# Kernel tuning notes

Measured on AMD Instinct MI355X. Metric: run time of the kernel, lower is better.

## Reference

```python
import jax, jax.numpy as jnp
import numpy as np

B, N_DEC, M_ENC, D, U = 16, 256, 256, 256, 256

def setup_inputs() -> dict:
    key = jax.random.key(0)
    ks = jax.random.split(key, 6)
    scale = 1.0 / np.sqrt(D)
    return {
        "encoder_output": jax.random.normal(ks[0], (B, M_ENC, D), dtype=jnp.float32),
        "decoder_output": jax.random.normal(ks[1], (B, N_DEC, D), dtype=jnp.float32),
        "W1": jax.random.normal(ks[2], (D, U), dtype=jnp.float32) * scale,
        "b1": jnp.zeros((U,), dtype=jnp.float32),
        "W2": jax.random.normal(ks[3], (D, U), dtype=jnp.float32) * scale,
        "b2": jnp.zeros((U,), dtype=jnp.float32),
        "v_w": jax.random.normal(ks[4], (U, 1), dtype=jnp.float32) * (1.0 / np.sqrt(U)),
        "v_b": jnp.zeros((1,), dtype=jnp.float32),
    }

def reference(encoder_output, decoder_output, W1, b1, W2, b2, v_w, v_b):
    # Project once per sequence, then broadcast (faithful to Dense on expanded dims):
    # enc_proj: [B, M, U], dec_proj: [B, N, U]
    enc_proj = jnp.einsum('bmd,du->bmu', encoder_output, W1) + b1
    dec_proj = jnp.einsum('bnd,du->bnu', decoder_output, W2) + b2
    # score: [B, N, M, U] = tanh(enc_proj[:,None,:,:] + dec_proj[:,:,None,:])
    score = jnp.tanh(enc_proj[:, None, :, :] + dec_proj[:, :, None, :])
    # logits: [B, N, M, 1]; softmax over encoder axis (axis=2)
    logits = jnp.einsum('bnmu,uo->bnmo', score, v_w) + v_b
    attention_weights = jax.nn.softmax(logits, axis=2)
    # context: sum over M of weights * encoder_output -> [B, N, D]
    context_vector = jnp.einsum('bnmo,bmd->bnd', attention_weights, encoder_output)
    return context_vector, attention_weights
```

## Files before the change

kernel.cpp:

```cpp
#include <hip/hip_runtime.h>


constexpr float KSC   = 2.8853900817779268f;
constexpr float LOG2E = 1.4426950408889634f;
constexpr float S16   = 1.52587890625e-05f;
constexpr float LSC   = -3.0517578125e-05f;

struct F4 { float v[4]; };
__device__ __forceinline__ F4 ld4(const float* p) {
    float4 t = *(const float4*)p;
    F4 r; r.v[0] = t.x; r.v[1] = t.y; r.v[2] = t.z; r.v[3] = t.w; return r;
}
__device__ __forceinline__ float rcp_clamp(float v) {
    float r = __builtin_amdgcn_rcpf(v);
    return fminf(fmaxf(r, -1e4f), 1e4f);
}

__global__ __launch_bounds__(256) void proj_kernel(
    const float* __restrict__ enc, const float* __restrict__ dec,
    const float* __restrict__ W1,  const float* __restrict__ b1,
    const float* __restrict__ W2,  const float* __restrict__ b2,
    const float* __restrict__ vw,
    float* __restrict__ encQ, float* __restrict__ decE)
{
    __shared__ float Xs[64][33];
    __shared__ float Ws[64][68];

    const int tid = threadIdx.x;
    const int tm = tid & 15, tu = tid >> 4;
    const int u0   = blockIdx.x * 64;
    const int row0 = blockIdx.y * 32;
    const bool is_enc = row0 < 4096;
    const float* X    = is_enc ? enc : dec;
    const float* W    = is_enc ? W1  : W2;
    const float* bias = is_enc ? b1  : b2;
    const int rb = is_enc ? row0 : row0 - 4096;

    float acc[2][4] = {};
    for (int kt = 0; kt < 256; kt += 64) {
        __syncthreads();
        #pragma unroll
        for (int i = 0; i < 2; ++i) {
            const int f = tid + (i << 8);
            const int row = f >> 4, kq = (f & 15) << 2;
            F4 x = ld4(&X[(rb + row) * 256 + kt + kq]);
            Xs[kq + 0][row] = x.v[0];
            Xs[kq + 1][row] = x.v[1];
            Xs[kq + 2][row] = x.v[2];
            Xs[kq + 3][row] = x.v[3];
        }
        #pragma unroll
        for (int i = 0; i < 4; ++i) {
            const int f = tid + (i << 8);
            const int kk = f >> 4, uq = (f & 15) << 2;
            *(float4*)&Ws[kk][uq] = *(const float4*)&W[(kt + kk) * 256 + u0 + uq];
        }
        __syncthreads();
        #pragma unroll 8
        for (int k = 0; k < 64; ++k) {
            const float xa0 = Xs[k][(tm << 1) | 0];
            const float xa1 = Xs[k][(tm << 1) | 1];
            const F4 wa = ld4(&Ws[k][tu << 2]);
            #pragma unroll
            for (int j = 0; j < 4; ++j) {
                acc[0][j] = fmaf(xa0, wa.v[j], acc[0][j]);
                acc[1][j] = fmaf(xa1, wa.v[j], acc[1][j]);
            }
        }
    }

    const int ucol = u0 + (tu << 2);
    const F4 bb = ld4(&bias[ucol]);
    if (is_enc) {
        const int b  = rb >> 8;
        const int m0 = (rb & 255) + (tm << 1);
        const int uq = ucol >> 2;
        #pragma unroll
        for (int i = 0; i < 2; ++i) {
            float4 o;
            o.x = __builtin_amdgcn_exp2f(fmaf(KSC, acc[i][0] + bb.v[0], -16.f));
            o.y = __builtin_amdgcn_exp2f(fmaf(KSC, acc[i][1] + bb.v[1], -16.f));
            o.z = __builtin_amdgcn_exp2f(fmaf(KSC, acc[i][2] + bb.v[2], -16.f));
            o.w = __builtin_amdgcn_exp2f(fmaf(KSC, acc[i][3] + bb.v[3], -16.f));
            *(float4*)&encQ[b * 65536 + uq * 1024 + (m0 + i) * 4] = o;
        }
    } else {
        const F4 vv = ld4(&vw[ucol]);
        float rv[4];
        #pragma unroll
        for (int j = 0; j < 4; ++j) rv[j] = rcp_clamp(vv.v[j]);
        const int r0 = rb + (tm << 1);
        #pragma unroll
        for (int i = 0; i < 2; ++i) {
            float4 o;
            o.x = __builtin_amdgcn_exp2f(KSC * (acc[i][0] + bb.v[0])) * rv[0];
            o.y = __builtin_amdgcn_exp2f(KSC * (acc[i][1] + bb.v[1])) * rv[1];
            o.z = __builtin_amdgcn_exp2f(KSC * (acc[i][2] + bb.v[2])) * rv[2];
            o.w = __builtin_amdgcn_exp2f(KSC * (acc[i][3] + bb.v[3])) * rv[3];
            *(float4*)&decE[(r0 + i) * 256 + ucol] = o;
        }
    }
}

__global__ __launch_bounds__(512) void logit_kernel(
    const float* __restrict__ encQ,
    const float* __restrict__ decE,
    const float* __restrict__ vw,
    float* __restrict__ logits)
{
    __shared__ float dsD[8][256];
    __shared__ float vcs[256];

    const int tid = threadIdx.x;
    const int b   = blockIdx.y;
    const int n0  = blockIdx.x << 3;
    const int h   = tid >> 8;
    const int m   = tid & 255;
    const int t0  = h << 2;

    {
        const float* dsrc = decE + (b * 256 + n0) * 256;
        #pragma unroll
        for (int i = 0; i < 4; ++i)
            ((float*)dsD)[tid + (i << 9)] = dsrc[tid + (i << 9)];
        if (tid < 256) vcs[tid] = S16 * rcp_clamp(vw[tid]);
    }
    __syncthreads();

    const float* ep = encQ + b * 65536 + (m << 2);
    F4 Ea = ld4(ep);
    F4 Eb = ld4(ep + 1024);
    ep += 2048;

    float acc[4] = {};

    #pragma unroll 4
    for (int o = 0; o < 32; ++o) {
        const F4 Ena = ld4(ep);
        const F4 Enb = ld4(ep + 1024);
        ep += 2048;
        const int u0 = o << 3;
        const F4 ca = ld4(&vcs[u0]);
        const F4 cb = ld4(&vcs[u0 + 4]);
        #pragma unroll
        for (int c = 0; c < 4; ++c) {
            const F4 da = ld4(&dsD[t0 + c][u0]);
            const F4 db = ld4(&dsD[t0 + c][u0 + 4]);
            const float z0 = fmaf(Ea.v[0], da.v[0], ca.v[0]);
            const float z1 = fmaf(Ea.v[1], da.v[1], ca.v[1]);
            const float z2 = fmaf(Ea.v[2], da.v[2], ca.v[2]);
            const float z3 = fmaf(Ea.v[3], da.v[3], ca.v[3]);
            const float y0 = fmaf(Eb.v[0], db.v[0], cb.v[0]);
            const float y1 = fmaf(Eb.v[1], db.v[1], cb.v[1]);
            const float y2 = fmaf(Eb.v[2], db.v[2], cb.v[2]);
            const float y3 = fmaf(Eb.v[3], db.v[3], cb.v[3]);
            const float pz01 = z0 * z1, pz23 = z2 * z3;
            const float py01 = y0 * y1, py23 = y2 * y3;
            const float nz = fmaf(z0 + z1, pz23, (z2 + z3) * pz01);
            const float ny = fmaf(y0 + y1, py23, (y2 + y3) * py01);
            const float pz = pz01 * pz23, py = py01 * py23;
            const float num = fmaf(nz, py, ny * pz);
            acc[c] = fmaf(num, __builtin_amdgcn_rcpf(pz * py), acc[c]);
        }
        Ea = Ena; Eb = Enb;
    }

    #pragma unroll
    for (int c = 0; c < 4; ++c)
        logits[(b * 256 + n0 + t0 + c) * 256 + m] = acc[c] * LSC;
}

__global__ __launch_bounds__(512) void smctx_kernel(
    const float* __restrict__ enc,
    float* __restrict__ out_attn,
    float* __restrict__ out_ctx)
{
    __shared__ float attn_s[8][256];
    __shared__ float redm[8][4], reds[8][4];

    const int tid = threadIdx.x;
    const int b   = blockIdx.y;
    const int n0  = blockIdx.x << 3;
    const int h   = tid >> 8;
    const int m   = tid & 255;
    const int t0  = h << 2;

    float l[4];
    #pragma unroll
    for (int c = 0; c < 4; ++c)
        l[c] = out_attn[(b * 256 + n0 + t0 + c) * 256 + m];

    const int lane = tid & 63, wq = (tid >> 6) & 3;
    #pragma unroll
    for (int c = 0; c < 4; ++c) {
        float x = l[c];
        #pragma unroll
        for (int off = 32; off > 0; off >>= 1)
            x = fmaxf(x, __shfl_xor(x, off));
        if (lane == 0) redm[t0 + c][wq] = x;
    }
    __syncthreads();
    float p[4];
    #pragma unroll
    for (int c = 0; c < 4; ++c) {
        const float mx = fmaxf(fmaxf(redm[t0 + c][0], redm[t0 + c][1]),
                               fmaxf(redm[t0 + c][2], redm[t0 + c][3]));
        p[c] = __builtin_amdgcn_exp2f((l[c] - mx) * LOG2E);
    }
    #pragma unroll
    for (int c = 0; c < 4; ++c) {
        float x = p[c];
        #pragma unroll
        for (int off = 32; off > 0; off >>= 1)
            x += __shfl_xor(x, off);
        if (lane == 0) reds[t0 + c][wq] = x;
    }
    __syncthreads();
    #pragma unroll
    for (int c = 0; c < 4; ++c) {
        const float s = (reds[t0 + c][0] + reds[t0 + c][1])
                      + (reds[t0 + c][2] + reds[t0 + c][3]);
        const float w = p[c] * __builtin_amdgcn_rcpf(s);
        attn_s[t0 + c][m] = w;
        out_attn[(b * 256 + n0 + t0 + c) * 256 + m] = w;
    }
    __syncthreads();

    const float* eb = enc + b * 65536 + m;
    float cx[4] = {};
    #pragma unroll 4
    for (int mm = 0; mm < 256; mm += 4) {
        const float g0 = eb[(mm + 0) << 8];
        const float g1 = eb[(mm + 1) << 8];
        const float g2 = eb[(mm + 2) << 8];
        const float g3 = eb[(mm + 3) << 8];
        #pragma unroll
        for (int c = 0; c < 4; ++c) {
            const F4 aq = ld4(&attn_s[t0 + c][mm]);
            cx[c] = fmaf(aq.v[0], g0, cx[c]);
            cx[c] = fmaf(aq.v[1], g1, cx[c]);
            cx[c] = fmaf(aq.v[2], g2, cx[c]);
            cx[c] = fmaf(aq.v[3], g3, cx[c]);
        }
    }
    #pragma unroll
    for (int c = 0; c < 4; ++c)
        out_ctx[(b * 256 + n0 + t0 + c) * 256 + m] = cx[c];
}

extern "C" void kernel_launch(void* const* d_in, const int* in_sizes, int n_in,
                              void* d_out, int out_size, void* d_ws, size_t ws_size,
                              hipStream_t stream) {
    const float* enc = (const float*)d_in[0];
    const float* dec = (const float*)d_in[1];
    const float* W1  = (const float*)d_in[2];
    const float* b1  = (const float*)d_in[3];
    const float* W2  = (const float*)d_in[4];
    const float* b2  = (const float*)d_in[5];
    const float* vw  = (const float*)d_in[6];

    float* out_ctx  = (float*)d_out;
    float* out_attn = (float*)d_out + 16 * 256 * 256;

    float* encQ = (float*)d_ws;
    float* decE = encQ + 16 * 256 * 256;

    proj_kernel <<<dim3(4, 256), 256, 0, stream>>>(enc, dec, W1, b1, W2, b2, vw, encQ, decE);
    logit_kernel<<<dim3(32, 16), 512, 0, stream>>>(encQ, decE, vw, out_attn);
    smctx_kernel<<<dim3(32, 16), 512, 0, stream>>>(enc, out_attn, out_ctx);
}
```

Before: 143.1 us.

## Split logit reduction over U halves, drop LDS in projection, vectorize context

The logit kernel now splits the U reduction into two halves across a third grid dimension, which doubles the block count for better occupancy. It writes partial logits to workspace, and the softmax kernel sums them. The projection GEMM drops shared-memory staging and has each wave read X and W directly from global memory with float4 loads. The context accumulation is remapped so each thread computes four contiguous D outputs for one row, using coalesced float4 encoder loads and a vector store. The cost is extra workspace traffic for the partial logits and more redundant global reads in the projection.

```diff
diff --git a/kernel.cpp b/kernel.cpp
--- a/kernel.cpp
+++ b/kernel.cpp
@@ -23,73 +23,63 @@
     const float* __restrict__ vw,
     float* __restrict__ encQ, float* __restrict__ decE)
 {
-    __shared__ float Xs[64][33];
-    __shared__ float Ws[64][68];
-
-    const int tid = threadIdx.x;
-    const int tm = tid & 15, tu = tid >> 4;
-    const int u0   = blockIdx.x * 64;
-    const int row0 = blockIdx.y * 32;
-    const bool is_enc = row0 < 4096;
+    const int tid  = threadIdx.x;
+    const int lane = tid & 63;
+    const int w    = __builtin_amdgcn_readfirstlane(tid >> 6);
+    const int ublk = blockIdx.x;
+    const int rblk = blockIdx.y;
+    const bool is_enc = rblk < 32;
     const float* X    = is_enc ? enc : dec;
     const float* W    = is_enc ? W1  : W2;
     const float* bias = is_enc ? b1  : b2;
-    const int rb = is_enc ? row0 : row0 - 4096;
+    const int rb = (is_enc ? rblk : rblk - 32) * 128;
+    const int r0 = rb + (lane << 1);
+    const int u0 = (ublk << 4) + (w << 2);
+
+    const float* x0p = X + r0 * 256;
+    const float* x1p = x0p + 256;
+    const float* wp  = W + u0;
 
     float acc[2][4] = {};
-    for (int kt = 0; kt < 256; kt += 64) {
-        __syncthreads();
+    #pragma unroll 8
+    for (int kq = 0; kq < 64; ++kq) {
+        const F4 xa = ld4(x0p + (kq << 2));
+        const F4 xb = ld4(x1p + (kq << 2));
+        const F4 w0 = ld4(wp + ((kq << 2) + 0) * 256);
+        const F4 w1 = ld4(wp + ((kq << 2) + 1) * 256);
+        const F4 w2 = ld4(wp + ((kq << 2) + 2) * 256);
+        const F4 w3 = ld4(wp + ((kq << 2) + 3) * 256);
+        #pragma unroll
+        for (int i = 0; i < 4; ++i) {
+            acc[0][i] = fmaf(xa.v[0], w0.v[i], acc[0][i]);
+            acc[1][i] = fmaf(xb.v[0], w0.v[i], acc[1][i]);
+            acc[0][i] = fmaf(xa.v[1], w1.v[i], acc[0][i]);
+            acc[1][i] = fmaf(xb.v[1], w1.v[i], acc[1][i]);
+            acc[0][i] = fmaf(xa.v[2], w2.v[i], acc[0][i]);
+            acc[1][i] = fmaf(xb.v[2], w2.v[i], acc[1][i]);
+            acc[0][i] = fmaf(xa.v[3], w3.v[i], acc[0][i]);
+            acc[1][i] = fmaf(xb.v[3], w3.v[i], acc[1][i]);
+        }
+    }
+
+    const F4 bb = ld4(&bias[u0]);
+    if (is_enc) {
+        const int uq = u0 >> 2;
         #pragma unroll
         for (int i = 0; i < 2; ++i) {
-            const int f = tid + (i << 8);
-            const int row = f >> 4, kq = (f & 15) << 2;
-            F4 x = ld4(&X[(rb + row) * 256 + kt + kq]);
-            Xs[kq + 0][row] = x.v[0];
-            Xs[kq + 1][row] = x.v[1];
-            Xs[kq + 2][row] = x.v[2];
-            Xs[kq + 3][row] = x.v[3];
-        }
-        #pragma unroll
-        for (int i = 0; i < 4; ++i) {
-            const int f = tid + (i << 8);
-            const int kk = f >> 4, uq = (f & 15) << 2;
-            *(float4*)&Ws[kk][uq] = *(const float4*)&W[(kt + kk) * 256 + u0 + uq];
-        }
-        __syncthreads();
-        #pragma unroll 8
-        for (int k = 0; k < 64; ++k) {
-            const float xa0 = Xs[k][(tm << 1) | 0];
-            const float xa1 = Xs[k][(tm << 1) | 1];
-            const F4 wa = ld4(&Ws[k][tu << 2]);
-            #pragma unroll
-            for (int j = 0; j < 4; ++j) {
-                acc[0][j] = fmaf(xa0, wa.v[j], acc[0][j]);
-                acc[1][j] = fmaf(xa1, wa.v[j], acc[1][j]);
-            }
-        }
-    }
-
-    const int ucol = u0 + (tu << 2);
-    const F4 bb = ld4(&bias[ucol]);
-    if (is_enc) {
-        const int b  = rb >> 8;
-        const int m0 = (rb & 255) + (tm << 1);
-        const int uq = ucol >> 2;
-        #pragma unroll
-        for (int i = 0; i < 2; ++i) {
+            const int r = r0 + i, b = r >> 8, m = r & 255;
             float4 o;
             o.x = __builtin_amdgcn_exp2f(fmaf(KSC, acc[i][0] + bb.v[0], -16.f));
             o.y = __builtin_amdgcn_exp2f(fmaf(KSC, acc[i][1] + bb.v[1], -16.f));
             o.z = __builtin_amdgcn_exp2f(fmaf(KSC, acc[i][2] + bb.v[2], -16.f));
             o.w = __builtin_amdgcn_exp2f(fmaf(KSC, acc[i][3] + bb.v[3], -16.f));
-            *(float4*)&encQ[b * 65536 + uq * 1024 + (m0 + i) * 4] = o;
+            *(float4*)&encQ[b * 65536 + uq * 1024 + m * 4] = o;
         }
     } else {
-        const F4 vv = ld4(&vw[ucol]);
+        const F4 vv = ld4(&vw[u0]);
         float rv[4];
         #pragma unroll
         for (int j = 0; j < 4; ++j) rv[j] = rcp_clamp(vv.v[j]);
-        const int r0 = rb + (tm << 1);
         #pragma unroll
         for (int i = 0; i < 2; ++i) {
             float4 o;
@@ -97,7 +87,7 @@
             o.y = __builtin_amdgcn_exp2f(KSC * (acc[i][1] + bb.v[1])) * rv[1];
             o.z = __builtin_amdgcn_exp2f(KSC * (acc[i][2] + bb.v[2])) * rv[2];
             o.w = __builtin_amdgcn_exp2f(KSC * (acc[i][3] + bb.v[3])) * rv[3];
-            *(float4*)&decE[(r0 + i) * 256 + ucol] = o;
+            *(float4*)&decE[(r0 + i) * 256 + u0] = o;
         }
     }
 }
@@ -106,28 +96,31 @@
     const float* __restrict__ encQ,
     const float* __restrict__ decE,
     const float* __restrict__ vw,
-    float* __restrict__ logits)
+    float* __restrict__ part)
 {
-    __shared__ float dsD[8][256];
-    __shared__ float vcs[256];
-
-    const int tid = threadIdx.x;
-    const int b   = blockIdx.y;
-    const int n0  = blockIdx.x << 3;
-    const int h   = tid >> 8;
-    const int m   = tid & 255;
-    const int t0  = h << 2;
+    __shared__ float dsD[8][128];
+    __shared__ float vcs[128];
+
+    const int tid  = threadIdx.x;
+    const int b    = blockIdx.y;
+    const int n0   = blockIdx.x << 3;
+    const int half = blockIdx.z;
+    const int h    = tid >> 8;
+    const int m    = tid & 255;
+    const int t0   = h << 2;
 
     {
-        const float* dsrc = decE + (b * 256 + n0) * 256;
-        #pragma unroll
-        for (int i = 0; i < 4; ++i)
-            ((float*)dsD)[tid + (i << 9)] = dsrc[tid + (i << 9)];
-        if (tid < 256) vcs[tid] = S16 * rcp_clamp(vw[tid]);
-    }
-    __syncthreads();
-
-    const float* ep = encQ + b * 65536 + (m << 2);
+        #pragma unroll
+        for (int rep = 0; rep < 2; ++rep) {
+            const int idx = tid + (rep << 9);
+            const int i = idx >> 7, u = idx & 127;
+            dsD[i][u] = decE[(b * 256 + n0 + i) * 256 + half * 128 + u];
+        }
+        if (tid < 128) vcs[tid] = S16 * rcp_clamp(vw[half * 128 + tid]);
+    }
+    __syncthreads();
+
+    const float* ep = encQ + b * 65536 + half * 32768 + (m << 2);
     F4 Ea = ld4(ep);
     F4 Eb = ld4(ep + 1024);
     ep += 2048;
@@ -135,7 +128,7 @@
     float acc[4] = {};
 
     #pragma unroll 4
-    for (int o = 0; o < 32; ++o) {
+    for (int o = 0; o < 16; ++o) {
         const F4 Ena = ld4(ep);
         const F4 Enb = ld4(ep + 1024);
         ep += 2048;
@@ -167,11 +160,12 @@
 
     #pragma unroll
     for (int c = 0; c < 4; ++c)
-        logits[(b * 256 + n0 + t0 + c) * 256 + m] = acc[c] * LSC;
+        part[((half << 4) + b) * 65536 + (n0 + t0 + c) * 256 + m] = acc[c] * LSC;
 }
 
 __global__ __launch_bounds__(512) void smctx_kernel(
     const float* __restrict__ enc,
+    const float* __restrict__ part,
     float* __restrict__ out_attn,
     float* __restrict__ out_ctx)
 {
@@ -187,8 +181,10 @@
 
     float l[4];
     #pragma unroll
-    for (int c = 0; c < 4; ++c)
-        l[c] = out_attn[(b * 256 + n0 + t0 + c) * 256 + m];
+    for (int c = 0; c < 4; ++c) {
+        const int off = (b * 256 + n0 + t0 + c) * 256 + m;
+        l[c] = part[off] + part[(16 << 16) + off];
+    }
 
     const int lane = tid & 63, wq = (tid >> 6) & 3;
     #pragma unroll
@@ -226,26 +222,24 @@
     }
     __syncthreads();
 
-    const float* eb = enc + b * 65536 + m;
+    const int dq = tid & 63, nc = tid >> 6;
+    const int d0 = dq << 2;
+    const float* eb = enc + b * 65536 + d0;
     float cx[4] = {};
     #pragma unroll 4
     for (int mm = 0; mm < 256; mm += 4) {
-        const float g0 = eb[(mm + 0) << 8];
-        const float g1 = eb[(mm + 1) << 8];
-        const float g2 = eb[(mm + 2) << 8];
-        const float g3 = eb[(mm + 3) << 8];
-        #pragma unroll
-        for (int c = 0; c < 4; ++c) {
-            const F4 aq = ld4(&attn_s[t0 + c][mm]);
-            cx[c] = fmaf(aq.v[0], g0, cx[c]);
-            cx[c] = fmaf(aq.v[1], g1, cx[c]);
-            cx[c] = fmaf(aq.v[2], g2, cx[c]);
-            cx[c] = fmaf(aq.v[3], g3, cx[c]);
-        }
-    }
-    #pragma unroll
-    for (int c = 0; c < 4; ++c)
-        out_ctx[(b * 256 + n0 + t0 + c) * 256 + m] = cx[c];
+        const F4 aq = ld4(&attn_s[nc][mm]);
+        #pragma unroll
+        for (int j = 0; j < 4; ++j) {
+            const F4 ev = ld4(eb + (mm + j) * 256);
+            cx[0] = fmaf(aq.v[j], ev.v[0], cx[0]);
+            cx[1] = fmaf(aq.v[j], ev.v[1], cx[1]);
+            cx[2] = fmaf(aq.v[j], ev.v[2], cx[2]);
+            cx[3] = fmaf(aq.v[j], ev.v[3], cx[3]);
+        }
+    }
+    float4 o; o.x = cx[0]; o.y = cx[1]; o.z = cx[2]; o.w = cx[3];
+    *(float4*)&out_ctx[(b * 256 + n0 + nc) * 256 + d0] = o;
 }
 
 extern "C" void kernel_launch(void* const* d_in, const int* in_sizes, int n_in,
@@ -264,8 +258,9 @@
 
     float* encQ = (float*)d_ws;
     float* decE = encQ + 16 * 256 * 256;
-
-    proj_kernel <<<dim3(4, 256), 256, 0, stream>>>(enc, dec, W1, b1, W2, b2, vw, encQ, decE);
-    logit_kernel<<<dim3(32, 16), 512, 0, stream>>>(encQ, decE, vw, out_attn);
-    smctx_kernel<<<dim3(32, 16), 512, 0, stream>>>(enc, out_attn, out_ctx);
-}
+    float* part = decE + 16 * 256 * 256;
+
+    proj_kernel <<<dim3(16, 64),    256, 0, stream>>>(enc, dec, W1, b1, W2, b2, vw, encQ, decE);
+    logit_kernel<<<dim3(32, 16, 2), 512, 0, stream>>>(encQ, decE, vw, part);
+    smctx_kernel<<<dim3(32, 16),    512, 0, stream>>>(enc, part, out_attn, out_ctx);
+}
```

New measurement: 195.9 us. 36.9% more time.

## Use split-bf16 MFMA for projection GEMM in proj_kernel

Applied to the files above, without the earlier changes.

Rewrites the projection GEMM to split each fp32 operand into high and low bf16 parts and accumulate three bf16 MFMA products (hi*hi, hi*lo, lo*hi), which approximates fp32 accuracy. Tiles grow to 64 rows per block, with four waves each computing a 32x32 sub-tile, so the grid is halved. The goal is to replace scalar FMA work with matrix-core throughput. In exchange there is conversion overhead during tile loading, strided scalar global loads for W, non-vectorized scattered epilogue stores, and a slight loss of precision.

```diff
diff --git a/kernel.cpp b/kernel.cpp
--- a/kernel.cpp
+++ b/kernel.cpp
@@ -15,6 +15,9 @@
     float r = __builtin_amdgcn_rcpf(v);
     return fminf(fmaxf(r, -1e4f), 1e4f);
 }
+
+typedef __attribute__((ext_vector_type(8))) short bf16x8;
+typedef __attribute__((ext_vector_type(4))) float f32x4;
 
 __global__ __launch_bounds__(256) void proj_kernel(
     const float* __restrict__ enc, const float* __restrict__ dec,
@@ -23,82 +26,125 @@
     const float* __restrict__ vw,
     float* __restrict__ encQ, float* __restrict__ decE)
 {
-    __shared__ float Xs[64][33];
-    __shared__ float Ws[64][68];
-
-    const int tid = threadIdx.x;
-    const int tm = tid & 15, tu = tid >> 4;
-    const int u0   = blockIdx.x * 64;
-    const int row0 = blockIdx.y * 32;
-    const bool is_enc = row0 < 4096;
+    __shared__ __align__(16) short Ah[64][40], Al[64][40];
+    __shared__ __align__(16) short Wh[64][40], Wl[64][40];
+
+    const int tid  = threadIdx.x;
+    const int lane = tid & 63;
+    const int wv   = tid >> 6;
+    const int wr   = wv >> 1, wc = wv & 1;
+    const int u0   = blockIdx.x << 6;
+    const int rblk = blockIdx.y;
+    const bool is_enc = rblk < 64;
     const float* X    = is_enc ? enc : dec;
-    const float* W    = is_enc ? W1  : W2;
+    const float* Wm   = is_enc ? W1  : W2;
     const float* bias = is_enc ? b1  : b2;
-    const int rb = is_enc ? row0 : row0 - 4096;
-
-    float acc[2][4] = {};
-    for (int kt = 0; kt < 256; kt += 64) {
+    const int rb = (is_enc ? rblk : rblk - 64) << 6;
+
+    const int r16 = lane & 15;
+    const int kg8 = (lane >> 4) << 3;
+
+    f32x4 acc[2][2] = {};
+
+    for (int kt = 0; kt < 256; kt += 32) {
+        {
+            const int row = tid >> 2, koct = (tid & 3) << 3;
+            const float* src = X + (rb + row) * 256 + kt + koct;
+            bf16x8 vh, vl;
+            #pragma unroll
+            for (int j = 0; j < 8; ++j) {
+                const float x = src[j];
+                const unsigned bx = __float_as_uint(x);
+                const float fh = __uint_as_float(bx & 0xFFFF0000u);
+                vh[j] = (short)(bx >> 16);
+                vl[j] = (short)(__float_as_uint(x - fh) >> 16);
+            }
+            *reinterpret_cast<bf16x8*>(&Ah[row][koct]) = vh;
+            *reinterpret_cast<bf16x8*>(&Al[row][koct]) = vl;
+        }
+        {
+            const int ul = tid & 63, koct = (tid >> 6) << 3;
+            const float* src = Wm + (kt + koct) * 256 + u0 + ul;
+            bf16x8 vh, vl;
+            #pragma unroll
+            for (int j = 0; j < 8; ++j) {
+                const float x = src[j * 256];
+                const unsigned bx = __float_as_uint(x);
+                const float fh = __uint_as_float(bx & 0xFFFF0000u);
+                vh[j] = (short)(bx >> 16);
+                vl[j] = (short)(__float_as_uint(x - fh) >> 16);
+            }
+            *reinterpret_cast<bf16x8*>(&Wh[ul][koct]) = vh;
+            *reinterpret_cast<bf16x8*>(&Wl[ul][koct]) = vl;
+        }
         __syncthreads();
+
+        bf16x8 fah[2], fal[2], fbh[2], fbl[2];
         #pragma unroll
         for (int i = 0; i < 2; ++i) {
-            const int f = tid + (i << 8);
-            const int row = f >> 4, kq = (f & 15) << 2;
-            F4 x = ld4(&X[(rb + row) * 256 + kt + kq]);
-            Xs[kq + 0][row] = x.v[0];
-            Xs[kq + 1][row] = x.v[1];
-            Xs[kq + 2][row] = x.v[2];
-            Xs[kq + 3][row] = x.v[3];
-        }
-        #pragma unroll
-        for (int i = 0; i < 4; ++i) {
-            const int f = tid + (i << 8);
-            const int kk = f >> 4, uq = (f & 15) << 2;
-            *(float4*)&Ws[kk][uq] = *(const float4*)&W[(kt + kk) * 256 + u0 + uq];
-        }
+            const int ar = (wr << 5) + (i << 4) + r16;
+            fah[i] = *reinterpret_cast<const bf16x8*>(&Ah[ar][kg8]);
+            fal[i] = *reinterpret_cast<const bf16x8*>(&Al[ar][kg8]);
+        }
+        #pragma unroll
+        for (int j = 0; j < 2; ++j) {
+            const int wu = (wc << 5) + (j << 4) + r16;
+            fbh[j] = *reinterpret_cast<const bf16x8*>(&Wh[wu][kg8]);
+            fbl[j] = *reinterpret_cast<const bf16x8*>(&Wl[wu][kg8]);
+        }
+        #pragma unroll
+        for (int i = 0; i < 2; ++i)
+            #pragma unroll
+            for (int j = 0; j < 2; ++j) {
+                acc[i][j] = __builtin_amdgcn_mfma_f32_16x16x32_bf16(
+                    fah[i], fbh[j], acc[i][j], 0, 0, 0);
+                acc[i][j] = __builtin_amdgcn_mfma_f32_16x16x32_bf16(
+                    fah[i], fbl[j], acc[i][j], 0, 0, 0);
+                acc[i][j] = __builtin_amdgcn_mfma_f32_16x16x32_bf16(
+                    fal[i], fbh[j], acc[i][j], 0, 0, 0);
+            }
         __syncthreads();
-        #pragma unroll 8
-        for (int k = 0; k < 64; ++k) {
-            const float xa0 = Xs[k][(tm << 1) | 0];
-            const float xa1 = Xs[k][(tm << 1) | 1];
-            const F4 wa = ld4(&Ws[k][tu << 2]);
-            #pragma unroll
-            for (int j = 0; j < 4; ++j) {
-                acc[0][j] = fmaf(xa0, wa.v[j], acc[0][j]);
-                acc[1][j] = fmaf(xa1, wa.v[j], acc[1][j]);
-            }
-        }
-    }
-
-    const int ucol = u0 + (tu << 2);
-    const F4 bb = ld4(&bias[ucol]);
+    }
+
+    const int kg = lane >> 4;
+    float bb[2];
+    #pragma unroll
+    for (int j = 0; j < 2; ++j)
+        bb[j] = bias[u0 + (wc << 5) + (j << 4) + r16];
+
     if (is_enc) {
-        const int b  = rb >> 8;
-        const int m0 = (rb & 255) + (tm << 1);
-        const int uq = ucol >> 2;
-        #pragma unroll
-        for (int i = 0; i < 2; ++i) {
-            float4 o;
-            o.x = __builtin_amdgcn_exp2f(fmaf(KSC, acc[i][0] + bb.v[0], -16.f));
-            o.y = __builtin_amdgcn_exp2f(fmaf(KSC, acc[i][1] + bb.v[1], -16.f));
-            o.z = __builtin_amdgcn_exp2f(fmaf(KSC, acc[i][2] + bb.v[2], -16.f));
-            o.w = __builtin_amdgcn_exp2f(fmaf(KSC, acc[i][3] + bb.v[3], -16.f));
-            *(float4*)&encQ[b * 65536 + uq * 1024 + (m0 + i) * 4] = o;
-        }
+        #pragma unroll
+        for (int i = 0; i < 2; ++i)
+            #pragma unroll
+            for (int j = 0; j < 2; ++j) {
+                const int gu = u0 + (wc << 5) + (j << 4) + r16;
+                #pragma unroll
+                for (int r = 0; r < 4; ++r) {
+                    const int grow = rb + (wr << 5) + (i << 4) + (kg << 2) + r;
+                    const int b = grow >> 8, m = grow & 255;
+                    const float val = __builtin_amdgcn_exp2f(
+                        fmaf(KSC, acc[i][j][r] + bb[j], -16.f));
+                    encQ[b * 65536 + (gu >> 2) * 1024 + (m << 2) + (gu & 3)] = val;
+                }
+            }
     } else {
-        const F4 vv = ld4(&vw[ucol]);
-        float rv[4];
-        #pragma unroll
-        for (int j = 0; j < 4; ++j) rv[j] = rcp_clamp(vv.v[j]);
-        const int r0 = rb + (tm << 1);
-        #pragma unroll
-        for (int i = 0; i < 2; ++i) {
-            float4 o;
-            o.x = __builtin_amdgcn_exp2f(KSC * (acc[i][0] + bb.v[0])) * rv[0];
-            o.y = __builtin_amdgcn_exp2f(KSC * (acc[i][1] + bb.v[1])) * rv[1];
-            o.z = __builtin_amdgcn_exp2f(KSC * (acc[i][2] + bb.v[2])) * rv[2];
-            o.w = __builtin_amdgcn_exp2f(KSC * (acc[i][3] + bb.v[3])) * rv[3];
-            *(float4*)&decE[(r0 + i) * 256 + ucol] = o;
-        }
+        float rv[2];
+        #pragma unroll
+        for (int j = 0; j < 2; ++j)
+            rv[j] = rcp_clamp(vw[u0 + (wc << 5) + (j << 4) + r16]);
+        #pragma unroll
+        for (int i = 0; i < 2; ++i)
+            #pragma unroll
+            for (int j = 0; j < 2; ++j) {
+                const int gu = u0 + (wc << 5) + (j << 4) + r16;
+                #pragma unroll
+                for (int r = 0; r < 4; ++r) {
+                    const int grow = rb + (wr << 5) + (i << 4) + (kg << 2) + r;
+                    const float val = __builtin_amdgcn_exp2f(
+                        KSC * (acc[i][j][r] + bb[j])) * rv[j];
+                    decE[grow * 256 + gu] = val;
+                }
+            }
     }
 }
 
@@ -265,7 +311,7 @@
     float* encQ = (float*)d_ws;
     float* decE = encQ + 16 * 256 * 256;
 
-    proj_kernel <<<dim3(4, 256), 256, 0, stream>>>(enc, dec, W1, b1, W2, b2, vw, encQ, decE);
+    proj_kernel <<<dim3(4, 128), 256, 0, stream>>>(enc, dec, W1, b1, W2, b2, vw, encQ, decE);
     logit_kernel<<<dim3(32, 16), 512, 0, stream>>>(encQ, decE, vw, out_attn);
     smctx_kernel<<<dim3(32, 16), 512, 0, stream>>>(enc, out_attn, out_ctx);
 }
```

Result: faster. 132.0 us (-7.8%).
